# Kernel optimization log

Hardware: AMD Instinct MI355X
Metric: run time of the kernel (lower is better)

The kernel has to match this reference:

```python
import jax, jax.numpy as jnp
import numpy as np

BLOCK_SIZE = 128


def setup_inputs() -> dict:
    key = jax.random.key(0)
    kq, kk, kv = jax.random.split(key, 3)
    b, t, e = 16, 8192, 256
    Q = jax.random.normal(kq, (b, t, e), dtype=jnp.float32)
    K = jax.random.normal(kk, (b, t, e), dtype=jnp.float32)
    V = jax.random.normal(kv, (b, t, e), dtype=jnp.float32)
    return {"Q": Q, "K": K, "V": V}


def reference(Q, K, V):
    b, t, e = Q.shape
    bs = BLOCK_SIZE
    n = t // bs
    scale = 1.0 / jnp.sqrt(jnp.asarray(e, Q.dtype))
    Qb = Q.reshape(b, n, bs, e)
    Kb = K.reshape(b, n, bs, e)
    Vb = V.reshape(b, n, bs, e)
    # block-diagonal scores: [b, n, bs, bs]
    Z = jnp.einsum('bnqe,bnke->bnqk', Qb, Kb) * scale
    causal = jnp.triu(jnp.ones((bs, bs), dtype=bool), k=1)  # True above diagonal
    Z = jnp.where(causal, -jnp.inf, Z)
    A = jax.nn.softmax(Z, axis=-1)
    out = jnp.einsum('bnqk,bnke->bnqe', A, Vb).reshape(b, t, e)
    A_flat = A.reshape(b, t, bs)  # matches torch view(b, t, block_size)
    return out, A_flat
```

## Files before the change

### kernel.cpp

```cpp
#include <hip/hip_runtime.h>

#define T_  8192
#define E_  256
#define BS_ 128

typedef __attribute__((ext_vector_type(8))) short bf16x8;
typedef __attribute__((ext_vector_type(4))) float f32x4;

__device__ __forceinline__ unsigned short f2bf(float x) {
    unsigned int u = __float_as_uint(x);
    u += 0x7fffu + ((u >> 16) & 1u);
    return (unsigned short)(u >> 16);
}

__device__ __forceinline__ bf16x8 pack8(f32x4 a, f32x4 b) {
    bf16x8 r;
    r[0] = (short)f2bf(a[0]); r[1] = (short)f2bf(a[1]);
    r[2] = (short)f2bf(a[2]); r[3] = (short)f2bf(a[3]);
    r[4] = (short)f2bf(b[0]); r[5] = (short)f2bf(b[1]);
    r[6] = (short)f2bf(b[2]); r[7] = (short)f2bf(b[3]);
    return r;
}

__device__ __forceinline__ void lds_barrier() {
    asm volatile("s_waitcnt lgkmcnt(0)" ::: "memory");
    __builtin_amdgcn_s_barrier();
}

__global__ __launch_bounds__(512, 4) void dba_fused(
        const float* __restrict__ Qg, const float* __restrict__ Kg,
        const float* __restrict__ Vg, float* __restrict__ Ag,
        float* __restrict__ Og)
{
    __shared__ unsigned short Sm[BS_ * E_];

    const int tid  = threadIdx.x;
    const int lane = tid & 63;
    const int w    = tid >> 6;
    const int cl   = lane & 15;
    const int g    = lane >> 4;
    const int bi   = blockIdx.x >> 6;
    const int ni   = blockIdx.x & 63;
    const int base  = (bi * T_ + ni * BS_) * E_;
    const int abase = (bi * T_ + ni * BS_) * BS_;
    const int vcol  = w * 32 + cl;

    const float* qp = Qg + base + (w * 16 + cl) * E_;
    f32x4 q0 = __builtin_nontemporal_load((const f32x4*)(qp + g * 8));
    f32x4 q1 = __builtin_nontemporal_load((const f32x4*)(qp + g * 8 + 4));

    {
        const int c4   = lane * 4;
        const int chnk = c4 >> 3;
        const int klow = c4 & 7;
        #pragma unroll 8
        for (int i = 0; i < 16; ++i) {
            const int n = i * 8 + w;
            f32x4 kv = __builtin_nontemporal_load((const f32x4*)(Kg + base + n * E_ + c4));
            const int cp = chnk ^ (n & 15);
            uint2 pk;
            pk.x = (unsigned)f2bf(kv[0]) | ((unsigned)f2bf(kv[1]) << 16);
            pk.y = (unsigned)f2bf(kv[2]) | ((unsigned)f2bf(kv[3]) << 16);
            *(uint2*)&Sm[n * E_ + cp * 8 + klow] = pk;
        }
    }
    lds_barrier();

    f32x4 acc[8];
    #pragma unroll
    for (int nt = 0; nt < 8; ++nt) acc[nt] = (f32x4){0.f, 0.f, 0.f, 0.f};

    for (int ks = 0; ks < 8; ++ks) {
        bf16x8 aq = pack8(q0, q1);
        if (ks < 7) {
            const int kn = (ks + 1) * 32 + g * 8;
            q0 = __builtin_nontemporal_load((const f32x4*)(qp + kn));
            q1 = __builtin_nontemporal_load((const f32x4*)(qp + kn + 4));
        }
        #pragma unroll
        for (int nt = 0; nt < 8; ++nt) {
            const int n  = nt * 16 + cl;
            const int cp = (ks * 4 + g) ^ cl;
            bf16x8 bk = *(const bf16x8*)&Sm[n * E_ + cp * 8];
            acc[nt] = __builtin_amdgcn_mfma_f32_16x16x32_bf16(aq, bk, acc[nt], 0, 0, 0);
        }
    }

    float vb[2][16];
    #pragma unroll
    for (int t = 0; t < 16; ++t)
        vb[0][t] = __builtin_nontemporal_load(
            Vg + base + (g * 8 + (t & 7)) * E_ + vcol + (t >> 3) * 16);
    #pragma unroll
    for (int t = 0; t < 16; ++t)
        vb[1][t] = __builtin_nontemporal_load(
            Vg + base + (32 + g * 8 + (t & 7)) * E_ + vcol + (t >> 3) * 16);

    const float scale = 0.0625f;
    const float L2E   = 1.4426950408889634f;
    #pragma unroll
    for (int r = 0; r < 4; ++r) {
        const int q = w * 16 + g * 4 + r;
        float m = -__builtin_inff();
        #pragma unroll
        for (int nt = 0; nt < 8; ++nt) {
            const int c = nt * 16 + cl;
            float z = acc[nt][r] * scale;
            z = (c > q) ? -__builtin_inff() : z;
            acc[nt][r] = z;
            m = fmaxf(m, z);
        }
        m = fmaxf(m, __shfl_xor(m, 1));
        m = fmaxf(m, __shfl_xor(m, 2));
        m = fmaxf(m, __shfl_xor(m, 4));
        m = fmaxf(m, __shfl_xor(m, 8));
        float s = 0.f;
        #pragma unroll
        for (int nt = 0; nt < 8; ++nt) {
            const float p = exp2f((acc[nt][r] - m) * L2E);
            acc[nt][r] = p;
            s += p;
        }
        s += __shfl_xor(s, 1);
        s += __shfl_xor(s, 2);
        s += __shfl_xor(s, 4);
        s += __shfl_xor(s, 8);
        const float rinv = __builtin_amdgcn_rcpf(s);
        #pragma unroll
        for (int nt = 0; nt < 8; ++nt)
            acc[nt][r] *= rinv;
    }

    #pragma unroll
    for (int nt = 0; nt < 8; ++nt)
        #pragma unroll
        for (int r = 0; r < 4; ++r)
            __builtin_nontemporal_store(acc[nt][r],
                Ag + abase + (w * 16 + g * 4 + r) * BS_ + nt * 16 + cl);

    lds_barrier();

    #pragma unroll
    for (int nt = 0; nt < 8; ++nt)
        #pragma unroll
        for (int r = 0; r < 4; ++r) {
            const int q = w * 16 + g * 4 + r;
            const int k = nt * 16 + cl;
            Sm[q * BS_ + (((k >> 3) ^ (g * 4 + r)) * 8) + (k & 7)] = f2bf(acc[nt][r]);
        }

    lds_barrier();

    f32x4 acc2[8][2];
    #pragma unroll
    for (int mt = 0; mt < 8; ++mt) {
        acc2[mt][0] = (f32x4){0.f, 0.f, 0.f, 0.f};
        acc2[mt][1] = (f32x4){0.f, 0.f, 0.f, 0.f};
    }

    #pragma unroll
    for (int ks = 0; ks < 4; ++ks) {
        bf16x8 bv0, bv1;
        #pragma unroll
        for (int j = 0; j < 8; ++j) {
            bv0[j] = (short)f2bf(vb[ks & 1][j]);
            bv1[j] = (short)f2bf(vb[ks & 1][8 + j]);
        }
        if (ks < 2) {
            #pragma unroll
            for (int t = 0; t < 16; ++t)
                vb[ks & 1][t] = __builtin_nontemporal_load(
                    Vg + base + ((ks + 2) * 32 + g * 8 + (t & 7)) * E_ + vcol + (t >> 3) * 16);
        }
        #pragma unroll
        for (int mt = 0; mt < 8; ++mt) {
            const int q = mt * 16 + cl;
            const bf16x8 pa = *(const bf16x8*)&Sm[q * BS_ + (((ks * 4 + g) ^ cl) * 8)];
            acc2[mt][0] = __builtin_amdgcn_mfma_f32_16x16x32_bf16(pa, bv0, acc2[mt][0], 0, 0, 0);
            acc2[mt][1] = __builtin_amdgcn_mfma_f32_16x16x32_bf16(pa, bv1, acc2[mt][1], 0, 0, 0);
        }
    }

    #pragma unroll
    for (int mt = 0; mt < 8; ++mt)
        #pragma unroll
        for (int n2 = 0; n2 < 2; ++n2)
            #pragma unroll
            for (int r = 0; r < 4; ++r)
                __builtin_nontemporal_store(acc2[mt][n2][r],
                    Og + base + (mt * 16 + g * 4 + r) * E_ + vcol + n2 * 16);
}

extern "C" void kernel_launch(void* const* d_in, const int* in_sizes, int n_in,
                              void* d_out, int out_size, void* d_ws, size_t ws_size,
                              hipStream_t stream) {
    const float* Q = (const float*)d_in[0];
    const float* K = (const float*)d_in[1];
    const float* V = (const float*)d_in[2];
    float* O = (float*)d_out;
    const int b = in_sizes[0] / (T_ * E_);
    float* A = O + (size_t)b * T_ * E_;
    dim3 grid(b * (T_ / BS_));
    dim3 block(512);
    dba_fused<<<grid, block, 0, stream>>>(Q, K, V, A, O);
}
```

Measured before the change: 444.6 us.

## Preload all Q and first V tiles before barrier, use hardware bf16 conversion

Loads the entire Q row slice (16 vector loads) and the first two V tiles up front, overlapping them with the K staging into LDS instead of streaming Q per k-step after the barrier. Replaces the manual round-to-nearest bf16 conversion with the compiler's __bf16 cast, which can lower to packed hardware conversion instructions. Also drops nontemporal hints on the loads. The extra live registers (64 floats for Q plus 32 for V) raise register pressure and may lower occupancy under the launch bounds.

```diff
diff --git a/kernel.cpp b/kernel.cpp
--- a/kernel.cpp
+++ b/kernel.cpp
@@ -6,20 +6,23 @@
 
 typedef __attribute__((ext_vector_type(8))) short bf16x8;
 typedef __attribute__((ext_vector_type(4))) float f32x4;
-
-__device__ __forceinline__ unsigned short f2bf(float x) {
-    unsigned int u = __float_as_uint(x);
-    u += 0x7fffu + ((u >> 16) & 1u);
-    return (unsigned short)(u >> 16);
+typedef __attribute__((ext_vector_type(4))) unsigned int u32x4;
+
+__device__ __forceinline__ unsigned pkbf(float a, float b) {
+    unsigned short ua = __builtin_bit_cast(unsigned short, (__bf16)a);
+    unsigned short ub = __builtin_bit_cast(unsigned short, (__bf16)b);
+    return (unsigned)ua | ((unsigned)ub << 16);
+}
+
+__device__ __forceinline__ unsigned short bf1(float a) {
+    return __builtin_bit_cast(unsigned short, (__bf16)a);
 }
 
 __device__ __forceinline__ bf16x8 pack8(f32x4 a, f32x4 b) {
-    bf16x8 r;
-    r[0] = (short)f2bf(a[0]); r[1] = (short)f2bf(a[1]);
-    r[2] = (short)f2bf(a[2]); r[3] = (short)f2bf(a[3]);
-    r[4] = (short)f2bf(b[0]); r[5] = (short)f2bf(b[1]);
-    r[6] = (short)f2bf(b[2]); r[7] = (short)f2bf(b[3]);
-    return r;
+    u32x4 u;
+    u[0] = pkbf(a[0], a[1]); u[1] = pkbf(a[2], a[3]);
+    u[2] = pkbf(b[0], b[1]); u[3] = pkbf(b[2], b[3]);
+    return __builtin_bit_cast(bf16x8, u);
 }
 
 __device__ __forceinline__ void lds_barrier() {
@@ -46,8 +49,10 @@
     const int vcol  = w * 32 + cl;
 
     const float* qp = Qg + base + (w * 16 + cl) * E_;
-    f32x4 q0 = __builtin_nontemporal_load((const f32x4*)(qp + g * 8));
-    f32x4 q1 = __builtin_nontemporal_load((const f32x4*)(qp + g * 8 + 4));
+    f32x4 qf[16];
+    #pragma unroll
+    for (int i = 0; i < 16; ++i)
+        qf[i] = *(const f32x4*)(qp + (i >> 1) * 32 + g * 8 + (i & 1) * 4);
 
     {
         const int c4   = lane * 4;
@@ -56,45 +61,44 @@
         #pragma unroll 8
         for (int i = 0; i < 16; ++i) {
             const int n = i * 8 + w;
-            f32x4 kv = __builtin_nontemporal_load((const f32x4*)(Kg + base + n * E_ + c4));
+            f32x4 kv = *(const f32x4*)(Kg + base + n * E_ + c4);
             const int cp = chnk ^ (n & 15);
             uint2 pk;
-            pk.x = (unsigned)f2bf(kv[0]) | ((unsigned)f2bf(kv[1]) << 16);
-            pk.y = (unsigned)f2bf(kv[2]) | ((unsigned)f2bf(kv[3]) << 16);
+            pk.x = pkbf(kv[0], kv[1]);
+            pk.y = pkbf(kv[2], kv[3]);
             *(uint2*)&Sm[n * E_ + cp * 8 + klow] = pk;
         }
     }
+
+    bf16x8 aq[8];
+    #pragma unroll
+    for (int ks = 0; ks < 8; ++ks)
+        aq[ks] = pack8(qf[2 * ks], qf[2 * ks + 1]);
+
+    float vb[2][16];
+    #pragma unroll
+    for (int t = 0; t < 16; ++t)
+        vb[0][t] = Vg[base + (g * 8 + (t & 7)) * E_ + vcol + (t >> 3) * 16];
+    #pragma unroll
+    for (int t = 0; t < 16; ++t)
+        vb[1][t] = Vg[base + (32 + g * 8 + (t & 7)) * E_ + vcol + (t >> 3) * 16];
+
     lds_barrier();
 
     f32x4 acc[8];
     #pragma unroll
     for (int nt = 0; nt < 8; ++nt) acc[nt] = (f32x4){0.f, 0.f, 0.f, 0.f};
 
+    #pragma unroll
     for (int ks = 0; ks < 8; ++ks) {
-        bf16x8 aq = pack8(q0, q1);
-        if (ks < 7) {
-            const int kn = (ks + 1) * 32 + g * 8;
-            q0 = __builtin_nontemporal_load((const f32x4*)(qp + kn));
-            q1 = __builtin_nontemporal_load((const f32x4*)(qp + kn + 4));
-        }
         #pragma unroll
         for (int nt = 0; nt < 8; ++nt) {
             const int n  = nt * 16 + cl;
             const int cp = (ks * 4 + g) ^ cl;
             bf16x8 bk = *(const bf16x8*)&Sm[n * E_ + cp * 8];
-            acc[nt] = __builtin_amdgcn_mfma_f32_16x16x32_bf16(aq, bk, acc[nt], 0, 0, 0);
-        }
-    }
-
-    float vb[2][16];
-    #pragma unroll
-    for (int t = 0; t < 16; ++t)
-        vb[0][t] = __builtin_nontemporal_load(
-            Vg + base + (g * 8 + (t & 7)) * E_ + vcol + (t >> 3) * 16);
-    #pragma unroll
-    for (int t = 0; t < 16; ++t)
-        vb[1][t] = __builtin_nontemporal_load(
-            Vg + base + (32 + g * 8 + (t & 7)) * E_ + vcol + (t >> 3) * 16);
+            acc[nt] = __builtin_amdgcn_mfma_f32_16x16x32_bf16(aq[ks], bk, acc[nt], 0, 0, 0);
+        }
+    }
 
     const float scale = 0.0625f;
     const float L2E   = 1.4426950408889634f;
@@ -146,7 +150,7 @@
         for (int r = 0; r < 4; ++r) {
             const int q = w * 16 + g * 4 + r;
             const int k = nt * 16 + cl;
-            Sm[q * BS_ + (((k >> 3) ^ (g * 4 + r)) * 8) + (k & 7)] = f2bf(acc[nt][r]);
+            Sm[q * BS_ + (((k >> 3) ^ (g * 4 + r)) * 8) + (k & 7)] = bf1(acc[nt][r]);
         }
 
     lds_barrier();
@@ -160,17 +164,16 @@
 
     #pragma unroll
     for (int ks = 0; ks < 4; ++ks) {
-        bf16x8 bv0, bv1;
-        #pragma unroll
-        for (int j = 0; j < 8; ++j) {
-            bv0[j] = (short)f2bf(vb[ks & 1][j]);
-            bv1[j] = (short)f2bf(vb[ks & 1][8 + j]);
-        }
+        f32x4 v0a = {vb[ks & 1][0],  vb[ks & 1][1],  vb[ks & 1][2],  vb[ks & 1][3]};
+        f32x4 v0b = {vb[ks & 1][4],  vb[ks & 1][5],  vb[ks & 1][6],  vb[ks & 1][7]};
+        f32x4 v1a = {vb[ks & 1][8],  vb[ks & 1][9],  vb[ks & 1][10], vb[ks & 1][11]};
+        f32x4 v1b = {vb[ks & 1][12], vb[ks & 1][13], vb[ks & 1][14], vb[ks & 1][15]};
+        bf16x8 bv0 = pack8(v0a, v0b);
+        bf16x8 bv1 = pack8(v1a, v1b);
         if (ks < 2) {
             #pragma unroll
             for (int t = 0; t < 16; ++t)
-                vb[ks & 1][t] = __builtin_nontemporal_load(
-                    Vg + base + ((ks + 2) * 32 + g * 8 + (t & 7)) * E_ + vcol + (t >> 3) * 16);
+                vb[ks & 1][t] = Vg[base + ((ks + 2) * 32 + g * 8 + (t & 7)) * E_ + vcol + (t >> 3) * 16];
         }
         #pragma unroll
         for (int mt = 0; mt < 8; ++mt) {
```

Result: slower. 476.1 us (+7.1%).

## Double threads per block and split score columns across wave pairs

Applied to the files above, without the earlier changes.

Moves from 512 to 1024 threads per block. Each pair of waves now shares a 16-row query tile, with each wave computing half the key columns. Row max and sum are reduced across the pair through small shared arrays and extra barriers. The PV stage gives each wave 16 output columns instead of 32. The aim is to cut per-thread register pressure and raise the number of waves in flight to hide global memory latency, at the cost of redundant Q loads, extra LDS reductions and more barriers.

```diff
diff --git a/kernel.cpp b/kernel.cpp
--- a/kernel.cpp
+++ b/kernel.cpp
@@ -27,25 +27,29 @@
     __builtin_amdgcn_s_barrier();
 }
 
-__global__ __launch_bounds__(512, 4) void dba_fused(
+__global__ __launch_bounds__(1024, 8) void dba_fused(
         const float* __restrict__ Qg, const float* __restrict__ Kg,
         const float* __restrict__ Vg, float* __restrict__ Ag,
         float* __restrict__ Og)
 {
     __shared__ unsigned short Sm[BS_ * E_];
+    __shared__ float RedM[2][BS_];
+    __shared__ float RedS[2][BS_];
 
     const int tid  = threadIdx.x;
     const int lane = tid & 63;
     const int w    = tid >> 6;
     const int cl   = lane & 15;
     const int g    = lane >> 4;
+    const int rt   = w >> 1;
+    const int h    = w & 1;
     const int bi   = blockIdx.x >> 6;
     const int ni   = blockIdx.x & 63;
     const int base  = (bi * T_ + ni * BS_) * E_;
     const int abase = (bi * T_ + ni * BS_) * BS_;
-    const int vcol  = w * 32 + cl;
-
-    const float* qp = Qg + base + (w * 16 + cl) * E_;
+    const int vcol  = w * 16 + cl;
+
+    const float* qp = Qg + base + (rt * 16 + cl) * E_;
     f32x4 q0 = __builtin_nontemporal_load((const f32x4*)(qp + g * 8));
     f32x4 q1 = __builtin_nontemporal_load((const f32x4*)(qp + g * 8 + 4));
 
@@ -53,9 +57,9 @@
         const int c4   = lane * 4;
         const int chnk = c4 >> 3;
         const int klow = c4 & 7;
-        #pragma unroll 8
-        for (int i = 0; i < 16; ++i) {
-            const int n = i * 8 + w;
+        #pragma unroll
+        for (int i = 0; i < 8; ++i) {
+            const int n = i * 16 + w;
             f32x4 kv = __builtin_nontemporal_load((const f32x4*)(Kg + base + n * E_ + c4));
             const int cp = chnk ^ (n & 15);
             uint2 pk;
@@ -66,9 +70,9 @@
     }
     lds_barrier();
 
-    f32x4 acc[8];
-    #pragma unroll
-    for (int nt = 0; nt < 8; ++nt) acc[nt] = (f32x4){0.f, 0.f, 0.f, 0.f};
+    f32x4 acc[4];
+    #pragma unroll
+    for (int j = 0; j < 4; ++j) acc[j] = (f32x4){0.f, 0.f, 0.f, 0.f};
 
     for (int ks = 0; ks < 8; ++ks) {
         bf16x8 aq = pack8(q0, q1);
@@ -78,117 +82,107 @@
             q1 = __builtin_nontemporal_load((const f32x4*)(qp + kn + 4));
         }
         #pragma unroll
-        for (int nt = 0; nt < 8; ++nt) {
-            const int n  = nt * 16 + cl;
+        for (int j = 0; j < 4; ++j) {
+            const int n  = (h * 4 + j) * 16 + cl;
             const int cp = (ks * 4 + g) ^ cl;
             bf16x8 bk = *(const bf16x8*)&Sm[n * E_ + cp * 8];
-            acc[nt] = __builtin_amdgcn_mfma_f32_16x16x32_bf16(aq, bk, acc[nt], 0, 0, 0);
-        }
-    }
-
-    float vb[2][16];
-    #pragma unroll
-    for (int t = 0; t < 16; ++t)
-        vb[0][t] = __builtin_nontemporal_load(
-            Vg + base + (g * 8 + (t & 7)) * E_ + vcol + (t >> 3) * 16);
-    #pragma unroll
-    for (int t = 0; t < 16; ++t)
-        vb[1][t] = __builtin_nontemporal_load(
-            Vg + base + (32 + g * 8 + (t & 7)) * E_ + vcol + (t >> 3) * 16);
+            acc[j] = __builtin_amdgcn_mfma_f32_16x16x32_bf16(aq, bk, acc[j], 0, 0, 0);
+        }
+    }
+
+    f32x4 vb[2][2];
+    #pragma unroll
+    for (int t = 0; t < 8; ++t)
+        vb[0][t >> 2][t & 3] = __builtin_nontemporal_load(
+            Vg + base + (g * 8 + t) * E_ + vcol);
+    #pragma unroll
+    for (int t = 0; t < 8; ++t)
+        vb[1][t >> 2][t & 3] = __builtin_nontemporal_load(
+            Vg + base + (32 + g * 8 + t) * E_ + vcol);
 
     const float scale = 0.0625f;
     const float L2E   = 1.4426950408889634f;
     #pragma unroll
     for (int r = 0; r < 4; ++r) {
-        const int q = w * 16 + g * 4 + r;
+        const int q = rt * 16 + g * 4 + r;
         float m = -__builtin_inff();
         #pragma unroll
-        for (int nt = 0; nt < 8; ++nt) {
-            const int c = nt * 16 + cl;
-            float z = acc[nt][r] * scale;
+        for (int j = 0; j < 4; ++j) {
+            const int c = (h * 4 + j) * 16 + cl;
+            float z = acc[j][r] * scale;
             z = (c > q) ? -__builtin_inff() : z;
-            acc[nt][r] = z;
+            acc[j][r] = z;
             m = fmaxf(m, z);
         }
         m = fmaxf(m, __shfl_xor(m, 1));
         m = fmaxf(m, __shfl_xor(m, 2));
         m = fmaxf(m, __shfl_xor(m, 4));
         m = fmaxf(m, __shfl_xor(m, 8));
+        if (cl == 0) RedM[h][q] = m;
+    }
+    lds_barrier();
+
+    #pragma unroll
+    for (int r = 0; r < 4; ++r) {
+        const int q = rt * 16 + g * 4 + r;
+        const float m = fmaxf(RedM[0][q], RedM[1][q]);
         float s = 0.f;
         #pragma unroll
-        for (int nt = 0; nt < 8; ++nt) {
-            const float p = exp2f((acc[nt][r] - m) * L2E);
-            acc[nt][r] = p;
+        for (int j = 0; j < 4; ++j) {
+            const float p = exp2f((acc[j][r] - m) * L2E);
+            acc[j][r] = p;
             s += p;
         }
         s += __shfl_xor(s, 1);
         s += __shfl_xor(s, 2);
         s += __shfl_xor(s, 4);
         s += __shfl_xor(s, 8);
-        const float rinv = __builtin_amdgcn_rcpf(s);
-        #pragma unroll
-        for (int nt = 0; nt < 8; ++nt)
-            acc[nt][r] *= rinv;
-    }
-
-    #pragma unroll
-    for (int nt = 0; nt < 8; ++nt)
-        #pragma unroll
-        for (int r = 0; r < 4; ++r)
-            __builtin_nontemporal_store(acc[nt][r],
-                Ag + abase + (w * 16 + g * 4 + r) * BS_ + nt * 16 + cl);
-
-    lds_barrier();
-
-    #pragma unroll
-    for (int nt = 0; nt < 8; ++nt)
-        #pragma unroll
-        for (int r = 0; r < 4; ++r) {
-            const int q = w * 16 + g * 4 + r;
-            const int k = nt * 16 + cl;
-            Sm[q * BS_ + (((k >> 3) ^ (g * 4 + r)) * 8) + (k & 7)] = f2bf(acc[nt][r]);
-        }
-
-    lds_barrier();
-
-    f32x4 acc2[8][2];
-    #pragma unroll
-    for (int mt = 0; mt < 8; ++mt) {
-        acc2[mt][0] = (f32x4){0.f, 0.f, 0.f, 0.f};
-        acc2[mt][1] = (f32x4){0.f, 0.f, 0.f, 0.f};
-    }
+        if (cl == 0) RedS[h][q] = s;
+    }
+    lds_barrier();
+
+    #pragma unroll
+    for (int r = 0; r < 4; ++r) {
+        const int q = rt * 16 + g * 4 + r;
+        const float rinv = __builtin_amdgcn_rcpf(RedS[0][q] + RedS[1][q]);
+        #pragma unroll
+        for (int j = 0; j < 4; ++j) {
+            const float p = acc[j][r] * rinv;
+            acc[j][r] = p;
+            const int k = (h * 4 + j) * 16 + cl;
+            __builtin_nontemporal_store(p, Ag + abase + q * BS_ + k);
+            Sm[q * BS_ + (((k >> 3) ^ (g * 4 + r)) * 8) + (k & 7)] = f2bf(p);
+        }
+    }
+    lds_barrier();
+
+    f32x4 acc2[8];
+    #pragma unroll
+    for (int mt = 0; mt < 8; ++mt) acc2[mt] = (f32x4){0.f, 0.f, 0.f, 0.f};
 
     #pragma unroll
     for (int ks = 0; ks < 4; ++ks) {
-        bf16x8 bv0, bv1;
-        #pragma unroll
-        for (int j = 0; j < 8; ++j) {
-            bv0[j] = (short)f2bf(vb[ks & 1][j]);
-            bv1[j] = (short)f2bf(vb[ks & 1][8 + j]);
-        }
+        bf16x8 bv = pack8(vb[ks & 1][0], vb[ks & 1][1]);
         if (ks < 2) {
             #pragma unroll
-            for (int t = 0; t < 16; ++t)
-                vb[ks & 1][t] = __builtin_nontemporal_load(
-                    Vg + base + ((ks + 2) * 32 + g * 8 + (t & 7)) * E_ + vcol + (t >> 3) * 16);
+            for (int t = 0; t < 8; ++t)
+                vb[ks & 1][t >> 2][t & 3] = __builtin_nontemporal_load(
+                    Vg + base + ((ks + 2) * 32 + g * 8 + t) * E_ + vcol);
         }
         #pragma unroll
         for (int mt = 0; mt < 8; ++mt) {
             const int q = mt * 16 + cl;
             const bf16x8 pa = *(const bf16x8*)&Sm[q * BS_ + (((ks * 4 + g) ^ cl) * 8)];
-            acc2[mt][0] = __builtin_amdgcn_mfma_f32_16x16x32_bf16(pa, bv0, acc2[mt][0], 0, 0, 0);
-            acc2[mt][1] = __builtin_amdgcn_mfma_f32_16x16x32_bf16(pa, bv1, acc2[mt][1], 0, 0, 0);
+            acc2[mt] = __builtin_amdgcn_mfma_f32_16x16x32_bf16(pa, bv, acc2[mt], 0, 0, 0);
         }
     }
 
     #pragma unroll
     for (int mt = 0; mt < 8; ++mt)
         #pragma unroll
-        for (int n2 = 0; n2 < 2; ++n2)
-            #pragma unroll
-            for (int r = 0; r < 4; ++r)
-                __builtin_nontemporal_store(acc2[mt][n2][r],
-                    Og + base + (mt * 16 + g * 4 + r) * E_ + vcol + n2 * 16);
+        for (int r = 0; r < 4; ++r)
+            __builtin_nontemporal_store(acc2[mt][r],
+                Og + base + (mt * 16 + g * 4 + r) * E_ + vcol);
 }
 
 extern "C" void kernel_launch(void* const* d_in, const int* in_sizes, int n_in,
@@ -201,6 +195,6 @@
     const int b = in_sizes[0] / (T_ * E_);
     float* A = O + (size_t)b * T_ * E_;
     dim3 grid(b * (T_ / BS_));
-    dim3 block(512);
+    dim3 block(1024);
     dba_fused<<<grid, block, 0, stream>>>(Q, K, V, A, O);
 }
```

New measurement: 469.6 us. +5.6%, slower.
